# Kernel optimization log

Hardware: AMD Instinct MI355X
Metric: run time of the kernel (lower is better)

## Reference

```python
import jax, jax.numpy as jnp
import numpy as np

N_NODES = 50000
N_EDGES = 800000
IN_FEAT = 256
OUT_FEAT = 256
NUM_RELS = 8
ALPHA = 0.5


def setup_inputs() -> dict:
    key = jax.random.key(0)
    k1, k2, k3, k4, k5, k6 = jax.random.split(key, 6)
    x = jax.random.normal(k1, (N_NODES, IN_FEAT), dtype=jnp.float32)
    edge_index = jax.random.randint(k2, (2, N_EDGES), 0, N_NODES, dtype=jnp.int64)
    edge_type = jax.random.randint(k3, (N_EDGES,), 0, NUM_RELS, dtype=jnp.int64)
    # Xavier-uniform-ish init for weights (scale per fan-in/fan-out)
    gain = float(np.sqrt(2.0))  # calculate_gain('relu')
    lim_w = gain * float(np.sqrt(6.0 / (IN_FEAT + OUT_FEAT)))
    weight = jax.random.uniform(k4, (NUM_RELS, IN_FEAT, OUT_FEAT), dtype=jnp.float32,
                                minval=-lim_w, maxval=lim_w)
    loop_weight = jax.random.uniform(k5, (IN_FEAT, OUT_FEAT), dtype=jnp.float32,
                                     minval=-lim_w, maxval=lim_w)
    h_bias = jnp.zeros((OUT_FEAT,), dtype=jnp.float32)
    return {"edge_index": edge_index, "x": x, "edge_type": edge_type,
            "weight": weight, "h_bias": h_bias, "loop_weight": loop_weight}


def reference(edge_index, x, edge_type, weight, h_bias, loop_weight):
    num_nodes = x.shape[0]
    src, dst = edge_index[0], edge_index[1]
    # Per-edge message msg_e = x[src_e] @ weight[edge_type_e].
    # Computed efficiently as num_rels dense GEMMs over all nodes, then a fused
    # (relation, src) gather — identical math, avoids (E, in, out) weight blowup.
    hx = jnp.einsum('ni,rio->rno', x, weight)          # (R, N, out)
    msg = hx[edge_type, src]                            # (E, out)
    agg = jax.ops.segment_sum(msg, dst, num_segments=num_nodes)  # (N, out)
    node_repr = agg * jnp.asarray(ALPHA, x.dtype) ** 0.5
    node_repr = node_repr + h_bias
    loop_message = x @ loop_weight                      # (N, out)
    node_repr = node_repr + loop_message * jnp.asarray(1.0 - ALPHA, x.dtype) ** 0.5
    # activation=None, dropout=0.0 (eval) -> identity
    return node_repr
```

## Files before the change

kernel.cpp:

```cpp
#include <hip/hip_runtime.h>

typedef __bf16 bf16x8 __attribute__((ext_vector_type(8)));
typedef float f32x4 __attribute__((ext_vector_type(4)));

static __device__ __forceinline__ unsigned short f2bf(float f) {
    unsigned u = __builtin_bit_cast(unsigned, f);
    u += 0x7FFFu + ((u >> 16) & 1u);
    return (unsigned short)(u >> 16);
}
static __device__ __forceinline__ float bf2f(unsigned short h) {
    return __builtin_bit_cast(float, ((unsigned)h) << 16);
}

#define GLOAD_LDS16(g, l)                                              \
    __builtin_amdgcn_global_load_lds(                                  \
        (const __attribute__((address_space(1))) unsigned int*)(g),    \
        (__attribute__((address_space(3))) unsigned int*)(l), 16, 0, 0)

__global__ __launch_bounds__(256) void rgcn_zero(unsigned* __restrict__ p, int n) {
    int i = blockIdx.x * 256 + threadIdx.x;
    if (i < n) p[i] = 0;
}

__global__ __launch_bounds__(256) void rgcn_hist(const int* __restrict__ ei,
                                                 unsigned* __restrict__ cnt, int E) {
    int e = blockIdx.x * 256 + threadIdx.x;
    if (e < E) atomicAdd(&cnt[ei[E + e]], 1u);
}

__global__ __launch_bounds__(1024) void rgcn_scan1(const unsigned* __restrict__ cnt,
                                                   unsigned* __restrict__ off,
                                                   unsigned* __restrict__ bsum, int n) {
    __shared__ unsigned ws[16];
    const int t = threadIdx.x, lane = t & 63, wv = t >> 6;
    int i = blockIdx.x * 1024 + t;
    unsigned v = (i < n) ? cnt[i] : 0;
    unsigned s = v;
    #pragma unroll
    for (int d = 1; d < 64; d <<= 1) {
        unsigned u = __shfl_up(s, d, 64);
        if (lane >= d) s += u;
    }
    if (lane == 63) ws[wv] = s;
    __syncthreads();
    if (wv == 0) {
        unsigned b = (lane < 16) ? ws[lane] : 0;
        unsigned sb = b;
        #pragma unroll
        for (int d = 1; d < 16; d <<= 1) {
            unsigned u = __shfl_up(sb, d, 64);
            if (lane >= d) sb += u;
        }
        if (lane < 16) ws[lane] = sb - b;
        if (lane == 15) bsum[blockIdx.x] = sb;
    }
    __syncthreads();
    if (i < n) off[i] = ws[wv] + (s - v);
}

__global__ __launch_bounds__(64) void rgcn_scan2(unsigned* __restrict__ bsum,
                                                 unsigned* __restrict__ bsumo,
                                                 unsigned* __restrict__ off, int nb, int n) {
    const int lane = threadIdx.x & 63;
    unsigned b = (lane < nb) ? bsum[lane] : 0;
    unsigned s = b;
    #pragma unroll
    for (int d = 1; d < 64; d <<= 1) {
        unsigned u = __shfl_up(s, d, 64);
        if (lane >= d) s += u;
    }
    if (lane < nb) bsumo[lane] = s - b;
    if (lane == 63) off[n] = s;
}

__global__ __launch_bounds__(256) void rgcn_scan3(unsigned* __restrict__ off,
                                                  const unsigned* __restrict__ bsumo,
                                                  unsigned* __restrict__ cur, int n) {
    int i = blockIdx.x * 256 + threadIdx.x;
    if (i < n) {
        unsigned v = off[i] + bsumo[i >> 10];
        off[i] = v;
        cur[i] = v;
    }
}

__global__ __launch_bounds__(256) void rgcn_scatter(const int* __restrict__ ei,
                                                    const int* __restrict__ et,
                                                    unsigned* __restrict__ cur,
                                                    unsigned* __restrict__ recs, int E) {
    int e = blockIdx.x * 256 + threadIdx.x;
    if (e < E) {
        int dst = ei[E + e];
        unsigned p = atomicAdd(&cur[dst], 1u);
        recs[p] = (unsigned)ei[e] | ((unsigned)et[e] << 16);
    }
}

__global__ __launch_bounds__(256) void rgcn_cvt(const float* __restrict__ x,
                                                unsigned short* __restrict__ Z, int M) {
    int w = (blockIdx.x * 256 + threadIdx.x) >> 6;
    int lane = threadIdx.x & 63;
    if (w >= M) return;
    float4 v = *(const float4*)(x + (size_t)w * 256 + lane * 4);
    ushort4 o;
    o.x = f2bf(v.x); o.y = f2bf(v.y); o.z = f2bf(v.z); o.w = f2bf(v.w);
    *(ushort4*)(Z + (size_t)w * 2304 + 2048 + lane * 4) = o;
}

__global__ __launch_bounds__(256) void rgcn_wbt(const float* __restrict__ w,
                                                const float* __restrict__ lw,
                                                unsigned short* __restrict__ wbT) {
    int kc = blockIdx.x * 256 + threadIdx.x;
    int n  = blockIdx.y;
    if (kc >= 2304) return;
    float v;
    if (kc < 2048) {
        int r = kc >> 8, k = kc & 255;
        v = w[((size_t)r * 256 + k) * 256 + n];
    } else {
        v = lw[(size_t)(kc - 2048) * 256 + n];
    }
    wbT[(size_t)n * 2304 + kc] = f2bf(v * 0.70710678118654752f);
}

__global__ __launch_bounds__(256) void rgcn_agg(const unsigned* __restrict__ recs,
                                                const unsigned* __restrict__ off,
                                                unsigned short* __restrict__ Z, int M) {
    int w = (blockIdx.x * 256 + threadIdx.x) >> 6;
    int lane = threadIdx.x & 63;
    if (w >= M) return;
    unsigned o0 = off[w], o1 = off[w + 1];
    f32x4 a0 = {}, a1 = {}, a2 = {}, a3 = {}, a4 = {}, a5 = {}, a6 = {}, a7 = {};

#define LOADF(rec, fv)                                                                 \
    {                                                                                  \
        const ushort4 v_ = *(const ushort4*)(Z + (size_t)((rec) & 0xFFFFu) * 2304 +    \
                                             2048 + lane * 4);                         \
        fv[0] = bf2f(v_.x); fv[1] = bf2f(v_.y); fv[2] = bf2f(v_.z); fv[3] = bf2f(v_.w);\
    }
#define ACCUM(rec, fv)                                                                 \
    switch ((rec) >> 16) {                                                             \
        case 0: a0 += fv; break; case 1: a1 += fv; break;                              \
        case 2: a2 += fv; break; case 3: a3 += fv; break;                              \
        case 4: a4 += fv; break; case 5: a5 += fv; break;                              \
        case 6: a6 += fv; break; default: a7 += fv; break;                             \
    }

    unsigned i = o0;
    for (; i + 8 <= o1; i += 8) {
        unsigned r0 = recs[i],     r1 = recs[i + 1], r2 = recs[i + 2], r3 = recs[i + 3];
        unsigned r4 = recs[i + 4], r5 = recs[i + 5], r6 = recs[i + 6], r7 = recs[i + 7];
        f32x4 f0, f1, f2, f3, f4, f5, f6, f7;
        LOADF(r0, f0); LOADF(r1, f1); LOADF(r2, f2); LOADF(r3, f3);
        LOADF(r4, f4); LOADF(r5, f5); LOADF(r6, f6); LOADF(r7, f7);
        ACCUM(r0, f0); ACCUM(r1, f1); ACCUM(r2, f2); ACCUM(r3, f3);
        ACCUM(r4, f4); ACCUM(r5, f5); ACCUM(r6, f6); ACCUM(r7, f7);
    }
    for (; i < o1; ++i) {
        unsigned r0 = recs[i];
        f32x4 f0;
        LOADF(r0, f0);
        ACCUM(r0, f0);
    }
#undef LOADF
#undef ACCUM

    unsigned short* zr = Z + (size_t)w * 2304 + lane * 4;
#define ST(rr, ax)                                                                     \
    {                                                                                  \
        ushort4 o_;                                                                    \
        o_.x = f2bf(ax[0]); o_.y = f2bf(ax[1]); o_.z = f2bf(ax[2]); o_.w = f2bf(ax[3]);\
        *(ushort4*)(zr + rr * 256) = o_;                                               \
    }
    ST(0, a0) ST(1, a1) ST(2, a2) ST(3, a3) ST(4, a4) ST(5, a5) ST(6, a6) ST(7, a7)
#undef ST
}

#define BM 64
#define BK 64

__global__ __launch_bounds__(256) void rgcn_gemm(
    const unsigned short* __restrict__ A,
    const unsigned short* __restrict__ Bt,
    float* __restrict__ out,
    const float* __restrict__ bias,
    int M)
{
    __shared__ char lds[8192 + 32768];
    char* Ab = lds;
    char* Bb = lds + 8192;

    const int tid  = threadIdx.x;
    const int lane = tid & 63;
    const int wid  = tid >> 6;
    const int wn   = wid * 64;
    const int m0   = blockIdx.x * BM;

    f32x4 acc[4][4] = {};

    for (int kt = 0; kt < 2304; kt += BK) {
        __syncthreads();
        #pragma unroll
        for (int it = 0; it < 2; ++it) {
            int o   = it * 4096 + tid * 16;
            int r   = o >> 7;
            int scb = (o & 127) ^ ((r & 7) << 4);
            int ga  = m0 + r; if (ga >= M) ga = M - 1;
            GLOAD_LDS16((const char*)A + (size_t)ga * 4608 + (size_t)kt * 2 + scb, Ab + o);
        }
        #pragma unroll
        for (int it = 0; it < 8; ++it) {
            int o   = it * 4096 + tid * 16;
            int r   = o >> 7;
            int scb = (o & 127) ^ ((r & 7) << 4);
            GLOAD_LDS16((const char*)Bt + (size_t)r * 4608 + (size_t)kt * 2 + scb, Bb + o);
        }
        __syncthreads();
        #pragma unroll
        for (int kk = 0; kk < 2; ++kk) {
            const int koff = kk * 32 + (lane >> 4) * 8;
            bf16x8 af[4], bfr[4];
            #pragma unroll
            for (int i = 0; i < 4; ++i) {
                int ar = i * 16 + (lane & 15);
                af[i] = *(const bf16x8*)(Ab + ((ar * 128 + koff * 2) ^ ((ar & 7) << 4)));
            }
            #pragma unroll
            for (int j = 0; j < 4; ++j) {
                int br = wn + j * 16 + (lane & 15);
                bfr[j] = *(const bf16x8*)(Bb + ((br * 128 + koff * 2) ^ ((br & 7) << 4)));
            }
            #pragma unroll
            for (int i = 0; i < 4; ++i)
                #pragma unroll
                for (int j = 0; j < 4; ++j)
                    acc[i][j] = __builtin_amdgcn_mfma_f32_16x16x32_bf16(af[i], bfr[j], acc[i][j], 0, 0, 0);
        }
    }

    const int col = lane & 15;
    const int r0  = (lane >> 4) * 4;
    #pragma unroll
    for (int i = 0; i < 4; ++i) {
        #pragma unroll
        for (int j = 0; j < 4; ++j) {
            int gn = wn + j * 16 + col;
            float bv = bias[gn];
            #pragma unroll
            for (int rr = 0; rr < 4; ++rr) {
                int gm = m0 + i * 16 + r0 + rr;
                if (gm < M) out[(size_t)gm * 256 + gn] = acc[i][j][rr] + bv;
            }
        }
    }
}

extern "C" void kernel_launch(void* const* d_in, const int* in_sizes, int n_in,
                              void* d_out, int out_size, void* d_ws, size_t ws_size,
                              hipStream_t stream) {
    const int*   edge_index = (const int*)d_in[0];
    const float* x          = (const float*)d_in[1];
    const int*   edge_type  = (const int*)d_in[2];
    const float* weight     = (const float*)d_in[3];
    const float* h_bias     = (const float*)d_in[4];
    const float* loop_w     = (const float*)d_in[5];
    float* out = (float*)d_out;

    const int M = in_sizes[1] / 256;
    const int E = in_sizes[2];

    char* ws = (char*)d_ws;
    size_t off_b = 0;
    unsigned short* Zcat = (unsigned short*)(ws + off_b);
    off_b += (((size_t)M * 2304 * 2) + 255) & ~(size_t)255;
    unsigned short* wbT = (unsigned short*)(ws + off_b);
    off_b += (((size_t)256 * 2304 * 2) + 255) & ~(size_t)255;
    unsigned* cnt = (unsigned*)(ws + off_b);
    off_b += (((size_t)(M + 1) * 4) + 255) & ~(size_t)255;
    unsigned* off = (unsigned*)(ws + off_b);
    off_b += (((size_t)(M + 1) * 4) + 255) & ~(size_t)255;
    unsigned* bsum = (unsigned*)(ws + off_b);
    off_b += 256;
    unsigned* bsumo = (unsigned*)(ws + off_b);
    off_b += 256;
    unsigned* recs = (unsigned*)(ws + off_b);

    const int nb = (M + 1023) / 1024;

    rgcn_zero<<<(M + 255) / 256, 256, 0, stream>>>(cnt, M);
    rgcn_hist<<<(E + 255) / 256, 256, 0, stream>>>(edge_index, cnt, E);
    rgcn_scan1<<<nb, 1024, 0, stream>>>(cnt, off, bsum, M);
    rgcn_scan2<<<1, 64, 0, stream>>>(bsum, bsumo, off, nb, M);
    rgcn_scan3<<<(M + 255) / 256, 256, 0, stream>>>(off, bsumo, cnt, M);
    rgcn_scatter<<<(E + 255) / 256, 256, 0, stream>>>(edge_index, edge_type, cnt, recs, E);

    rgcn_cvt<<<(M + 3) / 4, 256, 0, stream>>>(x, Zcat, M);
    rgcn_wbt<<<dim3(9, 256), 256, 0, stream>>>(weight, loop_w, wbT);

    rgcn_agg<<<(M + 3) / 4, 256, 0, stream>>>(recs, off, Zcat, M);

    rgcn_gemm<<<(M + BM - 1) / BM, 256, 0, stream>>>(Zcat, wbT, out, h_bias, M);
}
```

Baseline: 359.3 us.

## Double-buffer A tiles in GEMM and make aggregation grid-stride

The GEMM now keeps two LDS buffers for the A tile and prefetches the A chunk two steps ahead. Each step waits only on the older loads with vmcnt(2), so global-to-LDS traffic overlaps the MFMA work. B stays single-buffered and is reloaded between barriers, so B load latency is still exposed. Separately, the aggregation kernel switches to a persistent grid-stride loop over nodes with a fixed grid of 2560 blocks, cutting block launch overhead but possibly lowering load balance and occupancy.

```diff
diff --git a/kernel.cpp b/kernel.cpp
--- a/kernel.cpp
+++ b/kernel.cpp
@@ -126,11 +126,9 @@
 __global__ __launch_bounds__(256) void rgcn_agg(const unsigned* __restrict__ recs,
                                                 const unsigned* __restrict__ off,
                                                 unsigned short* __restrict__ Z, int M) {
-    int w = (blockIdx.x * 256 + threadIdx.x) >> 6;
-    int lane = threadIdx.x & 63;
-    if (w >= M) return;
-    unsigned o0 = off[w], o1 = off[w + 1];
-    f32x4 a0 = {}, a1 = {}, a2 = {}, a3 = {}, a4 = {}, a5 = {}, a6 = {}, a7 = {};
+    const int gw0  = (blockIdx.x * 256 + threadIdx.x) >> 6;
+    const int nw   = (gridDim.x * 256) >> 6;
+    const int lane = threadIdx.x & 63;
 
 #define LOADF(rec, fv)                                                                 \
     {                                                                                  \
@@ -146,38 +144,45 @@
         case 6: a6 += fv; break; default: a7 += fv; break;                             \
     }
 
-    unsigned i = o0;
-    for (; i + 8 <= o1; i += 8) {
-        unsigned r0 = recs[i],     r1 = recs[i + 1], r2 = recs[i + 2], r3 = recs[i + 3];
-        unsigned r4 = recs[i + 4], r5 = recs[i + 5], r6 = recs[i + 6], r7 = recs[i + 7];
-        f32x4 f0, f1, f2, f3, f4, f5, f6, f7;
-        LOADF(r0, f0); LOADF(r1, f1); LOADF(r2, f2); LOADF(r3, f3);
-        LOADF(r4, f4); LOADF(r5, f5); LOADF(r6, f6); LOADF(r7, f7);
-        ACCUM(r0, f0); ACCUM(r1, f1); ACCUM(r2, f2); ACCUM(r3, f3);
-        ACCUM(r4, f4); ACCUM(r5, f5); ACCUM(r6, f6); ACCUM(r7, f7);
-    }
-    for (; i < o1; ++i) {
-        unsigned r0 = recs[i];
-        f32x4 f0;
-        LOADF(r0, f0);
-        ACCUM(r0, f0);
+    for (int w = gw0; w < M; w += nw) {
+        unsigned o0 = off[w], o1 = off[w + 1];
+        f32x4 a0 = {}, a1 = {}, a2 = {}, a3 = {}, a4 = {}, a5 = {}, a6 = {}, a7 = {};
+
+        unsigned i = o0;
+        for (; i + 8 <= o1; i += 8) {
+            unsigned r0 = recs[i],     r1 = recs[i + 1], r2 = recs[i + 2], r3 = recs[i + 3];
+            unsigned r4 = recs[i + 4], r5 = recs[i + 5], r6 = recs[i + 6], r7 = recs[i + 7];
+            f32x4 f0, f1, f2, f3, f4, f5, f6, f7;
+            LOADF(r0, f0); LOADF(r1, f1); LOADF(r2, f2); LOADF(r3, f3);
+            LOADF(r4, f4); LOADF(r5, f5); LOADF(r6, f6); LOADF(r7, f7);
+            ACCUM(r0, f0); ACCUM(r1, f1); ACCUM(r2, f2); ACCUM(r3, f3);
+            ACCUM(r4, f4); ACCUM(r5, f5); ACCUM(r6, f6); ACCUM(r7, f7);
+        }
+        for (; i < o1; ++i) {
+            unsigned r0 = recs[i];
+            f32x4 f0;
+            LOADF(r0, f0);
+            ACCUM(r0, f0);
+        }
+
+        unsigned short* zr = Z + (size_t)w * 2304 + lane * 4;
+#define ST(rr, ax)                                                                     \
+        {                                                                              \
+            ushort4 o_;                                                                \
+            o_.x = f2bf(ax[0]); o_.y = f2bf(ax[1]);                                    \
+            o_.z = f2bf(ax[2]); o_.w = f2bf(ax[3]);                                    \
+            *(ushort4*)(zr + rr * 256) = o_;                                           \
+        }
+        ST(0, a0) ST(1, a1) ST(2, a2) ST(3, a3) ST(4, a4) ST(5, a5) ST(6, a6) ST(7, a7)
+#undef ST
     }
 #undef LOADF
 #undef ACCUM
-
-    unsigned short* zr = Z + (size_t)w * 2304 + lane * 4;
-#define ST(rr, ax)                                                                     \
-    {                                                                                  \
-        ushort4 o_;                                                                    \
-        o_.x = f2bf(ax[0]); o_.y = f2bf(ax[1]); o_.z = f2bf(ax[2]); o_.w = f2bf(ax[3]);\
-        *(ushort4*)(zr + rr * 256) = o_;                                               \
-    }
-    ST(0, a0) ST(1, a1) ST(2, a2) ST(3, a3) ST(4, a4) ST(5, a5) ST(6, a6) ST(7, a7)
-#undef ST
 }
 
 #define BM 64
 #define BK 64
+#define NCH 36
 
 __global__ __launch_bounds__(256) void rgcn_gemm(
     const unsigned short* __restrict__ A,
@@ -186,9 +191,10 @@
     const float* __restrict__ bias,
     int M)
 {
-    __shared__ char lds[8192 + 32768];
-    char* Ab = lds;
-    char* Bb = lds + 8192;
+    __shared__ char lds[8192 * 2 + 32768];
+    char* Ab0 = lds;
+    char* Ab1 = lds + 8192;
+    char* Bb  = lds + 16384;
 
     const int tid  = threadIdx.x;
     const int lane = tid & 63;
@@ -198,24 +204,35 @@
 
     f32x4 acc[4][4] = {};
 
-    for (int kt = 0; kt < 2304; kt += BK) {
-        __syncthreads();
+    auto stageA = [&](int chunk, char* dst) {
         #pragma unroll
         for (int it = 0; it < 2; ++it) {
             int o   = it * 4096 + tid * 16;
             int r   = o >> 7;
             int scb = (o & 127) ^ ((r & 7) << 4);
             int ga  = m0 + r; if (ga >= M) ga = M - 1;
-            GLOAD_LDS16((const char*)A + (size_t)ga * 4608 + (size_t)kt * 2 + scb, Ab + o);
-        }
+            GLOAD_LDS16((const char*)A + (size_t)ga * 4608 + (size_t)chunk * 128 + scb, dst + o);
+        }
+    };
+    auto stageB = [&](int chunk) {
         #pragma unroll
         for (int it = 0; it < 8; ++it) {
             int o   = it * 4096 + tid * 16;
             int r   = o >> 7;
             int scb = (o & 127) ^ ((r & 7) << 4);
-            GLOAD_LDS16((const char*)Bt + (size_t)r * 4608 + (size_t)kt * 2 + scb, Bb + o);
-        }
-        __syncthreads();
+            GLOAD_LDS16((const char*)Bt + (size_t)r * 4608 + (size_t)chunk * 128 + scb, Bb + o);
+        }
+    };
+
+    stageA(0, Ab0);
+    stageB(0);
+    stageA(1, Ab1);
+    asm volatile("s_waitcnt vmcnt(2)" ::: "memory");
+    __builtin_amdgcn_s_barrier();
+    __builtin_amdgcn_sched_barrier(0);
+
+    for (int t = 0; t < NCH; ++t) {
+        const char* Acur = (t & 1) ? Ab1 : Ab0;
         #pragma unroll
         for (int kk = 0; kk < 2; ++kk) {
             const int koff = kk * 32 + (lane >> 4) * 8;
@@ -223,7 +240,7 @@
             #pragma unroll
             for (int i = 0; i < 4; ++i) {
                 int ar = i * 16 + (lane & 15);
-                af[i] = *(const bf16x8*)(Ab + ((ar * 128 + koff * 2) ^ ((ar & 7) << 4)));
+                af[i] = *(const bf16x8*)(Acur + ((ar * 128 + koff * 2) ^ ((ar & 7) << 4)));
             }
             #pragma unroll
             for (int j = 0; j < 4; ++j) {
@@ -235,6 +252,17 @@
                 #pragma unroll
                 for (int j = 0; j < 4; ++j)
                     acc[i][j] = __builtin_amdgcn_mfma_f32_16x16x32_bf16(af[i], bfr[j], acc[i][j], 0, 0, 0);
+        }
+
+        if (t < NCH - 1) {
+            __builtin_amdgcn_s_barrier();
+            __builtin_amdgcn_sched_barrier(0);
+            stageB(t + 1);
+            int tA = (t + 2 < NCH) ? t + 2 : NCH - 1;
+            stageA(tA, (t & 1) ? Ab1 : Ab0);
+            asm volatile("s_waitcnt vmcnt(2)" ::: "memory");
+            __builtin_amdgcn_s_barrier();
+            __builtin_amdgcn_sched_barrier(0);
         }
     }
 
@@ -297,7 +325,7 @@
     rgcn_cvt<<<(M + 3) / 4, 256, 0, stream>>>(x, Zcat, M);
     rgcn_wbt<<<dim3(9, 256), 256, 0, stream>>>(weight, loop_w, wbT);
 
-    rgcn_agg<<<(M + 3) / 4, 256, 0, stream>>>(recs, off, Zcat, M);
+    rgcn_agg<<<2560, 256, 0, stream>>>(recs, off, Zcat, M);
 
     rgcn_gemm<<<(M + BM - 1) / BM, 256, 0, stream>>>(Zcat, wbT, out, h_bias, M);
 }
```

Result: faster. 343.9 us (-4.3%).
